# Kernel tuning notes

Hardware: AMD Instinct MI355X
Metric: run time of the kernel (lower is better)

Reference implementation:

```python
import jax, jax.numpy as jnp
import numpy as np

B, S, L = 4, 1024, 512          # batch, max_seqlen, actual per-seq length
H, D = 12, 64                   # heads, head_dim
DIM = H * D                     # 768
NNZ = B * L                     # 2048 unpadded tokens


def setup_inputs() -> dict:
    key = jax.random.key(0)
    k1, k2, k3 = jax.random.split(key, 3)
    hidden_states = jax.random.normal(k1, (NNZ, DIM), jnp.float32)
    Wqkv_w = jax.random.normal(k2, (3 * DIM, DIM), jnp.float32) * 0.02
    Wqkv_b = jnp.zeros((3 * DIM,), jnp.float32)
    # ALiBi-style bias; in the real model it also encodes the padding mask (-inf),
    # here random values suffice for a correctness baseline.
    bias = jax.random.normal(k3, (B, H, S, S), jnp.float32) * 0.1
    # each sequence occupies the first L slots of its row in the padded layout
    indices = (jnp.arange(B)[:, None] * S + jnp.arange(L)[None, :]).reshape(-1).astype(jnp.int32)
    cu_seqlens = (jnp.arange(B + 1) * L).astype(jnp.int32)
    attn_mask = jnp.zeros((B, S), jnp.int32).at[:, :L].set(1)
    return dict(hidden_states=hidden_states, Wqkv_w=Wqkv_w, Wqkv_b=Wqkv_b,
                bias=bias, indices=indices, attn_mask=attn_mask,
                cu_seqlens=cu_seqlens, max_seqlen_in_batch=S)


def reference(hidden_states, Wqkv_w, Wqkv_b, bias, indices, attn_mask,
              cu_seqlens, max_seqlen_in_batch):
    b = attn_mask.shape[0]
    s = max_seqlen_in_batch
    # QKV projection on unpadded tokens: (nnz, 3*dim)
    qkv = hidden_states @ Wqkv_w.T + Wqkv_b
    # pad_input: scatter unpadded rows into (b*s) padded layout
    padded = jnp.zeros((b * s, qkv.shape[-1]), qkv.dtype).at[indices].set(qkv)
    qkv = padded.reshape(b, s, 3, H, D)
    q, k, v = qkv[:, :, 0], qkv[:, :, 1], qkv[:, :, 2]  # (b, s, h, d)
    scale = 1.0 / float(np.sqrt(D))
    scores = jnp.einsum('bqhd,bkhd->bhqk', q, k) * scale + bias  # (b,h,s,s)
    probs = jax.nn.softmax(scores, axis=-1)
    ctx = jnp.einsum('bhqk,bkhd->bqhd', probs, v)  # (b, s, h, d)
    # unpad_input_only: gather back rows where attn_mask == 1 (== indices)
    return ctx.reshape(b * s, H * D)[indices]
```

## Files before the change

kernel.cpp:

```cpp
#include <hip/hip_runtime.h>
#include <hip/hip_bf16.h>
#include <cstdint>

typedef short  s16x8 __attribute__((ext_vector_type(8)));
typedef ushort u16x8 __attribute__((ext_vector_type(8)));
typedef ushort u16x4 __attribute__((ext_vector_type(4)));
typedef float  f32x4 __attribute__((ext_vector_type(4)));

#define B_    4
#define S_    1024
#define H_    12
#define D_    64
#define DIM_  768
#define QSCALE 0.18033688011112042f
#define LOG2E  1.4426950408889634f

#define NTAIL 384

__device__ __forceinline__ ushort f2bf(float f) {
    __bf16 h = (__bf16)f;
    return __builtin_bit_cast(ushort, h);
}

__device__ __forceinline__ u16x8 cvt8(f32x4 x, f32x4 y) {
    u16x8 r;
    r[0]=f2bf(x[0]); r[1]=f2bf(x[1]); r[2]=f2bf(x[2]); r[3]=f2bf(x[3]);
    r[4]=f2bf(y[0]); r[5]=f2bf(y[1]); r[6]=f2bf(y[2]); r[7]=f2bf(y[3]);
    return r;
}

__global__ __launch_bounds__(256) void gemm_tail(
    const float* __restrict__ hidden, const float* __restrict__ W,
    const float* __restrict__ bvec, const float* __restrict__ bias,
    const int* __restrict__ cu,
    ushort* __restrict__ Qu, ushort* __restrict__ Ku, ushort* __restrict__ Vt,
    float* __restrict__ T, int ngemm, int nrows, int nnz)
{
    const int t = threadIdx.x;

    if ((int)blockIdx.x >= ngemm) {
        const int blk = blockIdx.x - ngemm;
        const int w = t >> 6, l = t & 63, grp = l >> 4, lc = l & 15;
        for (int rid = blk*16 + w*4 + grp; rid < nrows; rid += NTAIL*16) {
            const int h = rid / nnz;
            const int u = rid - h * nnz;
            int b = 0;
            while (cu[b+1] <= u) b++;
            const int q  = u - cu[b];
            const int Lb = cu[b+1] - cu[b];
            const float* rp = bias + ((size_t)(b*H_ + h)*S_ + q)*S_;
            float s = 0.0f;
            for (int k = Lb + lc*4; k < S_; k += 64) {
                f32x4 v = *(const f32x4*)(rp + k);
                s += exp2f(v[0]*LOG2E) + exp2f(v[1]*LOG2E)
                   + exp2f(v[2]*LOG2E) + exp2f(v[3]*LOG2E);
            }
            s += __shfl_xor(s, 1, 64);
            s += __shfl_xor(s, 2, 64);
            s += __shfl_xor(s, 4, 64);
            s += __shfl_xor(s, 8, 64);
            if (lc == 0) T[(size_t)(b*H_ + h)*S_ + q] = s;
        }
        return;
    }

    __shared__ ushort As[128][40];
    __shared__ ushort Bs[128][40];

    const int n0 = (blockIdx.x % 18) * 128;
    const int m0 = (blockIdx.x / 18) * 128;
    const int w  = t >> 6, l = t & 63, lg = l >> 4, lc = l & 15;
    const int wm = w >> 1, wn = w & 1;

    const int srow = t >> 1, shalf = t & 1;
    const float* aSrc = hidden + (size_t)(m0 + srow) * DIM_ + shalf * 16;
    const float* bSrc = W      + (size_t)(n0 + srow) * DIM_ + shalf * 16;

    f32x4 acc[4][4];
    #pragma unroll
    for (int i = 0; i < 4; i++)
        #pragma unroll
        for (int j = 0; j < 4; j++) acc[i][j] = (f32x4)0.0f;

    for (int k0 = 0; k0 < DIM_; k0 += 32) {
        __syncthreads();
        {
            const f32x4* a4 = (const f32x4*)(aSrc + k0);
            f32x4 x0 = a4[0], x1 = a4[1], x2 = a4[2], x3 = a4[3];
            const f32x4* b4 = (const f32x4*)(bSrc + k0);
            f32x4 y0 = b4[0], y1 = b4[1], y2 = b4[2], y3 = b4[3];
            *(u16x8*)&As[srow][shalf*16]     = cvt8(x0, x1);
            *(u16x8*)&As[srow][shalf*16 + 8] = cvt8(x2, x3);
            *(u16x8*)&Bs[srow][shalf*16]     = cvt8(y0, y1);
            *(u16x8*)&Bs[srow][shalf*16 + 8] = cvt8(y2, y3);
        }
        __syncthreads();
        s16x8 af[4], bfr[4];
        #pragma unroll
        for (int mi = 0; mi < 4; mi++)
            af[mi] = *(const s16x8*)&As[wm*64 + mi*16 + lc][lg*8];
        #pragma unroll
        for (int ni = 0; ni < 4; ni++)
            bfr[ni] = *(const s16x8*)&Bs[wn*64 + ni*16 + lc][lg*8];
        #pragma unroll
        for (int mi = 0; mi < 4; mi++)
            #pragma unroll
            for (int ni = 0; ni < 4; ni++)
                acc[mi][ni] = __builtin_amdgcn_mfma_f32_16x16x32_bf16(
                                  af[mi], bfr[ni], acc[mi][ni], 0, 0, 0);
    }

    const int sec = n0 / DIM_;
    float bv[4];
    #pragma unroll
    for (int ni = 0; ni < 4; ni++) bv[ni] = bvec[n0 + wn*64 + ni*16 + lc];

    #pragma unroll
    for (int mi = 0; mi < 4; mi++) {
        const int r = m0 + wm*64 + mi*16 + lg*4;
        if (sec == 2) {
            int b = 0;
            while (cu[b+1] <= r) b++;
            const int q = r - cu[b];
            #pragma unroll
            for (int ni = 0; ni < 4; ni++) {
                const int nl = wn*64 + ni*16 + lc + (n0 - 2*DIM_);
                const int h = nl >> 6, d = nl & 63;
                u16x4 pk;
                #pragma unroll
                for (int j = 0; j < 4; j++) pk[j] = f2bf(acc[mi][ni][j] + bv[ni]);
                *(u16x4*)&Vt[((size_t)((b*H_ + h)*64 + d))*S_ + q] = pk;
            }
        } else {
            #pragma unroll
            for (int j = 0; j < 4; j++) {
                #pragma unroll
                for (int ni = 0; ni < 4; ni++) {
                    const int nl = wn*64 + ni*16 + lc + (n0 - sec*DIM_);
                    float v = acc[mi][ni][j] + bv[ni];
                    if (sec == 0) Qu[(size_t)(r+j)*DIM_ + nl] = f2bf(v * QSCALE);
                    else          Ku[(size_t)(r+j)*DIM_ + nl] = f2bf(v);
                }
            }
        }
    }
}

__global__ __launch_bounds__(256) void attn_kernel(
    const ushort* __restrict__ Qu, const ushort* __restrict__ Ku,
    const ushort* __restrict__ Vt, const float* __restrict__ bias,
    const float* __restrict__ T, const int* __restrict__ cu,
    float* __restrict__ out)
{
    const int b  = blockIdx.x >> 4, qt = blockIdx.x & 15;
    const int h  = blockIdx.y;
    const int cu0 = cu[b];
    const int Lb  = cu[b+1] - cu0;
    const int qbase = qt * 64;
    if (qbase >= Lb) return;

    const int t = threadIdx.x, w = t >> 6, l = t & 63, lg = l >> 4, lc = l & 15;

    __shared__ ushort Ks[64][72];
    __shared__ ushort Vs[80][72];
    __shared__ ushort Ps[4][16][72];

    for (int i = t; i < 16*9; i += 256) {
        const int row = 64 + i/9, ch = i%9;
        u16x8 v = (u16x8)0;
        if (row == 64 && ch < 8)
            #pragma unroll
            for (int e = 0; e < 8; e++) v[e] = 0x3F80;
        *(u16x8*)&Vs[row][ch*8] = v;
    }

    const float*  bias_b = bias + (size_t)(b*H_ + h)*S_*S_;
    const ushort* kbase  = Ku + (size_t)cu0*DIM_ + h*64;
    const ushort* vbase  = Vt + (size_t)((b*H_ + h)*64)*S_;

    const int krow = t >> 3, kch = t & 7;

    const int rl = w*16 + lg*4;
    int p_[4]; bool val_[4];
    const float* bpr[4];
    #pragma unroll
    for (int j = 0; j < 4; j++) {
        const int r = qbase + rl + j;
        val_[j] = (r < Lb);
        p_[j]   = val_[j] ? r : (Lb - 1);
        bpr[j]  = bias_b + (size_t)p_[j]*S_;
    }

    int qar = qbase + w*16 + lc; if (qar >= Lb) qar = Lb - 1;
    const ushort* qp = Qu + (size_t)(cu0 + qar)*DIM_ + h*64;
    s16x8 qa0 = *(const s16x8*)(qp + lg*8);
    s16x8 qa1 = *(const s16x8*)(qp + 32 + lg*8);

    f32x4 O[4], lsum;
    #pragma unroll
    for (int d = 0; d < 4; d++) O[d] = (f32x4)0.0f;
    lsum = (f32x4)0.0f;

    float pf[4][4];
    u16x8 kr[2], vr[2];
    #pragma unroll
    for (int f = 0; f < 4; f++)
        #pragma unroll
        for (int j = 0; j < 4; j++) pf[f][j] = bpr[j][f*16 + lc];
    #pragma unroll
    for (int i = 0; i < 2; i++) {
        const int r = krow + i*32;
        const int rc = (r < Lb) ? r : Lb - 1;
        kr[i] = *(const u16x8*)(kbase + (size_t)rc*DIM_ + kch*8);
        vr[i] = *(const u16x8*)(vbase + (size_t)r*S_ + kch*8);
    }

    for (int k0 = 0; k0 < Lb; k0 += 64) {
        __syncthreads();
        #pragma unroll
        for (int i = 0; i < 2; i++) {
            const int r = krow + i*32;
            u16x8 kz = (k0 + r < Lb) ? kr[i] : (u16x8)0;
            *(u16x8*)&Ks[r][kch*8] = kz;
            *(u16x8*)&Vs[r][kch*8] = vr[i];
        }
        __syncthreads();

        f32x4 sc[4];
        #pragma unroll
        for (int f = 0; f < 4; f++)
            #pragma unroll
            for (int j = 0; j < 4; j++) sc[f][j] = pf[f][j] * LOG2E;

        const int kn = k0 + 64;
        if (kn < Lb) {
            #pragma unroll
            for (int f = 0; f < 4; f++)
                #pragma unroll
                for (int j = 0; j < 4; j++) pf[f][j] = bpr[j][kn + f*16 + lc];
            #pragma unroll
            for (int i = 0; i < 2; i++) {
                const int r = krow + i*32;
                const int rc = (kn + r < Lb) ? kn + r : Lb - 1;
                kr[i] = *(const u16x8*)(kbase + (size_t)rc*DIM_ + kch*8);
                vr[i] = *(const u16x8*)(vbase + (size_t)r*S_ + kn + kch*8);
            }
        }

        #pragma unroll
        for (int f = 0; f < 4; f++) {
            s16x8 kb0 = *(const s16x8*)&Ks[f*16 + lc][lg*8];
            s16x8 kb1 = *(const s16x8*)&Ks[f*16 + lc][32 + lg*8];
            sc[f] = __builtin_amdgcn_mfma_f32_16x16x32_bf16(qa0, kb0, sc[f], 0,0,0);
            sc[f] = __builtin_amdgcn_mfma_f32_16x16x32_bf16(qa1, kb1, sc[f], 0,0,0);
        }
        if (k0 + 64 > Lb) {
            #pragma unroll
            for (int f = 0; f < 4; f++) {
                const int kcol = k0 + f*16 + lc;
                if (kcol >= Lb)
                    #pragma unroll
                    for (int j = 0; j < 4; j++) sc[f][j] = -1e30f;
            }
        }

        #pragma unroll
        for (int f = 0; f < 4; f++)
            #pragma unroll
            for (int j = 0; j < 4; j++)
                Ps[w][lg*4 + j][f*16 + lc] = f2bf(exp2f(sc[f][j]));

        s16x8 pa0 = *(const s16x8*)&Ps[w][lc][lg*8];
        s16x8 pa1 = *(const s16x8*)&Ps[w][lc][32 + lg*8];
        #pragma unroll
        for (int df = 0; df < 4; df++) {
            s16x8 vb0 = *(const s16x8*)&Vs[df*16 + lc][lg*8];
            s16x8 vb1 = *(const s16x8*)&Vs[df*16 + lc][32 + lg*8];
            O[df] = __builtin_amdgcn_mfma_f32_16x16x32_bf16(pa0, vb0, O[df], 0,0,0);
            O[df] = __builtin_amdgcn_mfma_f32_16x16x32_bf16(pa1, vb1, O[df], 0,0,0);
        }
        {
            s16x8 ob0 = *(const s16x8*)&Vs[64 + lc][lg*8];
            s16x8 ob1 = *(const s16x8*)&Vs[64 + lc][32 + lg*8];
            lsum = __builtin_amdgcn_mfma_f32_16x16x32_bf16(pa0, ob0, lsum, 0,0,0);
            lsum = __builtin_amdgcn_mfma_f32_16x16x32_bf16(pa1, ob1, lsum, 0,0,0);
        }
    }

    #pragma unroll
    for (int j = 0; j < 4; j++) {
        float lj = lsum[j] + T[(size_t)(b*H_ + h)*S_ + p_[j]];
        float inv = 1.0f / lj;
        inv = __shfl(inv, l & 48, 64);
        if (val_[j]) {
            float* op = out + (size_t)(cu0 + qbase + rl + j)*DIM_ + h*64;
            #pragma unroll
            for (int df = 0; df < 4; df++) op[df*16 + lc] = O[df][j] * inv;
        }
    }
}

extern "C" void kernel_launch(void* const* d_in, const int* in_sizes, int n_in,
                              void* d_out, int out_size, void* d_ws, size_t ws_size,
                              hipStream_t stream)
{
    const float* hidden  = (const float*)d_in[0];
    const float* W       = (const float*)d_in[1];
    const float* bvec    = (const float*)d_in[2];
    const float* bias    = (const float*)d_in[3];
    const int*   cu      = (const int*)d_in[6];
    float*       out     = (float*)d_out;

    const int NNZ   = in_sizes[0] / DIM_;
    const int ngemm = 18 * (NNZ / 128);
    const int nrows = NNZ * H_;

    char* ws = (char*)d_ws;
    const size_t uB  = (size_t)NNZ * DIM_ * 2;
    const size_t vtB = (size_t)B_ * H_ * 64 * S_ * 2;
    ushort* Qu = (ushort*)(ws);
    ushort* Ku = (ushort*)(ws + uB);
    ushort* Vt = (ushort*)(ws + 2*uB);
    float*  T  = (float*)(ws + 2*uB + vtB);

    gemm_tail<<<ngemm + NTAIL, 256, 0, stream>>>(hidden, W, bvec, bias, cu,
                                                 Qu, Ku, Vt, T, ngemm, nrows, NNZ);

    dim3 ga(B_*(S_/64), H_);
    attn_kernel<<<ga, 256, 0, stream>>>(Qu, Ku, Vt, bias, T, cu, out);
}
```

Before: 62.33 us.

## Double K-tile to 64 and prefetch next tile into registers in QKV GEMM

The QKV projection GEMM main loop now stages a 64-wide K slice per iteration instead of 32, halving the number of barrier pairs. It also software-pipelines the loop: global loads for the next K slice are issued into registers before the MFMAs on the current shared tile, then converted and stored after a barrier. This hides global load latency behind compute. The cost is more registers (16 prefetch vectors plus 8 fragments), which may reduce occupancy, and a larger LDS footprint.

```diff
diff --git a/kernel.cpp b/kernel.cpp
--- a/kernel.cpp
+++ b/kernel.cpp
@@ -64,8 +64,8 @@
         return;
     }
 
-    __shared__ ushort As[128][40];
-    __shared__ ushort Bs[128][40];
+    __shared__ ushort As[128][72];
+    __shared__ ushort Bs[128][72];
 
     const int n0 = (blockIdx.x % 18) * 128;
     const int m0 = (blockIdx.x / 18) * 128;
@@ -73,8 +73,8 @@
     const int wm = w >> 1, wn = w & 1;
 
     const int srow = t >> 1, shalf = t & 1;
-    const float* aSrc = hidden + (size_t)(m0 + srow) * DIM_ + shalf * 16;
-    const float* bSrc = W      + (size_t)(n0 + srow) * DIM_ + shalf * 16;
+    const float* aSrc = hidden + (size_t)(m0 + srow) * DIM_ + shalf * 32;
+    const float* bSrc = W      + (size_t)(n0 + srow) * DIM_ + shalf * 32;
 
     f32x4 acc[4][4];
     #pragma unroll
@@ -82,32 +82,56 @@
         #pragma unroll
         for (int j = 0; j < 4; j++) acc[i][j] = (f32x4)0.0f;
 
-    for (int k0 = 0; k0 < DIM_; k0 += 32) {
-        __syncthreads();
-        {
-            const f32x4* a4 = (const f32x4*)(aSrc + k0);
-            f32x4 x0 = a4[0], x1 = a4[1], x2 = a4[2], x3 = a4[3];
-            const f32x4* b4 = (const f32x4*)(bSrc + k0);
-            f32x4 y0 = b4[0], y1 = b4[1], y2 = b4[2], y3 = b4[3];
-            *(u16x8*)&As[srow][shalf*16]     = cvt8(x0, x1);
-            *(u16x8*)&As[srow][shalf*16 + 8] = cvt8(x2, x3);
-            *(u16x8*)&Bs[srow][shalf*16]     = cvt8(y0, y1);
-            *(u16x8*)&Bs[srow][shalf*16 + 8] = cvt8(y2, y3);
-        }
-        __syncthreads();
-        s16x8 af[4], bfr[4];
+    f32x4 pa[8], pb[8];
+    #pragma unroll
+    for (int i = 0; i < 8; i++) {
+        pa[i] = *(const f32x4*)(aSrc + i*4);
+        pb[i] = *(const f32x4*)(bSrc + i*4);
+    }
+    #pragma unroll
+    for (int i = 0; i < 4; i++) {
+        *(u16x8*)&As[srow][shalf*32 + i*8] = cvt8(pa[2*i], pa[2*i+1]);
+        *(u16x8*)&Bs[srow][shalf*32 + i*8] = cvt8(pb[2*i], pb[2*i+1]);
+    }
+    __syncthreads();
+
+    for (int k0 = 0; k0 < DIM_; k0 += 64) {
+        const bool more = (k0 + 64 < DIM_);
+        if (more) {
+            #pragma unroll
+            for (int i = 0; i < 8; i++) {
+                pa[i] = *(const f32x4*)(aSrc + k0 + 64 + i*4);
+                pb[i] = *(const f32x4*)(bSrc + k0 + 64 + i*4);
+            }
+        }
+        s16x8 af[2][4], bfr[2][4];
+        #pragma unroll
+        for (int kk = 0; kk < 2; kk++) {
+            #pragma unroll
+            for (int mi = 0; mi < 4; mi++)
+                af[kk][mi] = *(const s16x8*)&As[wm*64 + mi*16 + lc][kk*32 + lg*8];
+            #pragma unroll
+            for (int ni = 0; ni < 4; ni++)
+                bfr[kk][ni] = *(const s16x8*)&Bs[wn*64 + ni*16 + lc][kk*32 + lg*8];
+        }
         #pragma unroll
         for (int mi = 0; mi < 4; mi++)
-            af[mi] = *(const s16x8*)&As[wm*64 + mi*16 + lc][lg*8];
-        #pragma unroll
-        for (int ni = 0; ni < 4; ni++)
-            bfr[ni] = *(const s16x8*)&Bs[wn*64 + ni*16 + lc][lg*8];
-        #pragma unroll
-        for (int mi = 0; mi < 4; mi++)
-            #pragma unroll
-            for (int ni = 0; ni < 4; ni++)
+            #pragma unroll
+            for (int ni = 0; ni < 4; ni++) {
                 acc[mi][ni] = __builtin_amdgcn_mfma_f32_16x16x32_bf16(
-                                  af[mi], bfr[ni], acc[mi][ni], 0, 0, 0);
+                                  af[0][mi], bfr[0][ni], acc[mi][ni], 0, 0, 0);
+                acc[mi][ni] = __builtin_amdgcn_mfma_f32_16x16x32_bf16(
+                                  af[1][mi], bfr[1][ni], acc[mi][ni], 0, 0, 0);
+            }
+        if (more) {
+            __syncthreads();
+            #pragma unroll
+            for (int i = 0; i < 4; i++) {
+                *(u16x8*)&As[srow][shalf*32 + i*8] = cvt8(pa[2*i], pa[2*i+1]);
+                *(u16x8*)&Bs[srow][shalf*32 + i*8] = cvt8(pb[2*i], pb[2*i+1]);
+            }
+            __syncthreads();
+        }
     }
 
     const int sec = n0 / DIM_;
```

After: 83.21 us. 1.34x slower.
